# Kernel optimization log

Measured on AMD Instinct MI355X. Metric: run time of the kernel, lower is better.

The kernel has to match this reference:

```python
import jax, jax.numpy as jnp
import numpy as np

B, C, H, W = 8, 256, 64, 64
CR = C // 4  # reduced channels for Q/K


def setup_inputs() -> dict:
    key = jax.random.key(0)
    ks = jax.random.split(key, 6)
    return {
        "source": jax.random.normal(ks[0], (B, C, H, W), dtype=jnp.float32),
        "guidance": jax.random.normal(ks[1], (B, C, H, W), dtype=jnp.float32),
        "Wq": jax.random.normal(ks[2], (CR, C), dtype=jnp.float32) * 0.02,
        "Wk": jax.random.normal(ks[3], (CR, C), dtype=jnp.float32) * 0.02,
        "Wv": jax.random.normal(ks[4], (C, C), dtype=jnp.float32) * 0.02,
        "bv": jax.random.normal(ks[5], (C,), dtype=jnp.float32) * 0.02,
        "gamma": jnp.zeros((1,), dtype=jnp.float32),
    }


def reference(source, guidance, Wq, Wk, Wv, bv, gamma):
    b, c, h, w = source.shape
    n = h * w
    src = source.reshape(b, c, n)       # [B,C,N]
    gui = guidance.reshape(b, c, n)     # [B,C,N]
    # 1x1 convs == per-pixel linear projections over channels
    Q = jnp.einsum('qc,bcn->bqn', Wq, src)                 # [B,CR,N]
    K = jnp.einsum('qc,bcn->bqn', Wk, gui)                 # [B,CR,N]
    V = jnp.einsum('vc,bcn->bvn', Wv, gui) + bv[None, :, None]  # [B,C,N]
    # energy[b,n,m] = sum_q Q[b,q,n] K[b,q,m]  (unscaled)
    energy = jnp.einsum('bqn,bqm->bnm', Q, K)              # [B,N,N]
    attn = jax.nn.softmax(energy, axis=-1)                 # softmax over keys m
    # out[b,c,n] = sum_m V[b,c,m] attn[b,n,m]
    out = jnp.einsum('bcm,bnm->bcn', V, attn)              # [B,C,N]
    return gamma[0] * out.reshape(b, c, h, w) + source
```

## Files before the change

kernel.cpp:

```cpp
#include <hip/hip_runtime.h>
#include <hip/hip_bf16.h>
#include <stdint.h>


#define B_ 8
#define C_ 256
#define N_ 4096
#define CR_ 64

typedef unsigned short u16;
typedef __attribute__((ext_vector_type(8))) __bf16 bf16x8;
typedef __attribute__((ext_vector_type(4))) float f32x4;
typedef __attribute__((ext_vector_type(16))) float f32x16;

__device__ __forceinline__ u16 f2bf(float f) {
  union { float f; unsigned int u; } v; v.f = f;
  unsigned int r = (v.u + 0x7fffu + ((v.u >> 16) & 1u)) >> 16;
  return (u16)r;
}
__device__ __forceinline__ unsigned int cvtpk(float a, float b) {
  unsigned int r;
  asm("v_cvt_pk_bf16_f32 %0, %1, %2" : "=v"(r) : "v"(a), "v"(b));
  return r;
}

typedef __attribute__((address_space(1))) const unsigned int gu32_t;
typedef __attribute__((address_space(3))) unsigned int lu32_t;
__device__ __forceinline__ void gll16(const void* g, void* l) {
  __builtin_amdgcn_global_load_lds((gu32_t*)g, (lu32_t*)l, 16, 0, 0);
}

__global__ __launch_bounds__(256) void wprep_kernel(
    const float* __restrict__ Wq, const float* __restrict__ Wk,
    const float* __restrict__ Wv, u16* __restrict__ Wb)
{
  const int i = (blockIdx.x * 256 + threadIdx.x) * 4;
  const int row = i >> 8;
  float4 v;
  float s = 1.0f;
  if (row < 64)       { v = *(const float4*)(Wq + i); s = 1.44269504f; }
  else if (row < 128) { v = *(const float4*)(Wk + i - 64 * 256); }
  else                { v = *(const float4*)(Wv + i - 128 * 256); }
  u16* o = Wb + i;
  o[0] = f2bf(v.x * s); o[1] = f2bf(v.y * s);
  o[2] = f2bf(v.z * s); o[3] = f2bf(v.w * s);
}

#define TSTR 266
#define LOAD_TILE(INP, BB, PX0) do {                                         \
    const int p4_ = (t & 15) * 4, r_ = t >> 4;                               \
    const float* ip_ = (INP) + (size_t)(BB) * C_ * N_ + (PX0) + p4_;         \
    for (int k = 0; k < 16; ++k) {                                           \
      const int c_ = r_ + k * 16;                                            \
      float4 v_ = *(const float4*)(ip_ + (size_t)c_ * N_);                   \
      Tl[(p4_ + 0) * TSTR + c_] = f2bf(v_.x);                                \
      Tl[(p4_ + 1) * TSTR + c_] = f2bf(v_.y);                                \
      Tl[(p4_ + 2) * TSTR + c_] = f2bf(v_.z);                                \
      Tl[(p4_ + 3) * TSTR + c_] = f2bf(v_.w);                                \
    }                                                                        \
  } while (0)

__global__ __launch_bounds__(256) void projqk_kernel(
    const float* __restrict__ src, const float* __restrict__ gui,
    const u16* __restrict__ Wb, u16* __restrict__ Qb, u16* __restrict__ Kb)
{
  __shared__ u16 Tl[64 * TSTR];
  const int t = threadIdx.x, lane = t & 63, wave = t >> 6;
  const int lg = lane >> 4, lm = lane & 15;
  const int b = blockIdx.y;
  const int role = blockIdx.z;
  const float* in = role ? gui : src;
  const u16* W64 = Wb + role * 64 * 256;
  u16* dst = role ? Kb : Qb;

  LOAD_TILE(in, b, blockIdx.x * 64);
  __syncthreads();

  f32x4 acc[4];
  const f32x4 z4 = {0.f, 0.f, 0.f, 0.f};
#pragma unroll
  for (int i = 0; i < 4; ++i) acc[i] = z4;

  for (int ks = 0; ks < 8; ++ks) {
    bf16x8 wf = *(const bf16x8*)(W64 + (wave * 16 + lm) * C_ + ks * 32 + lg * 8);
#pragma unroll
    for (int ni = 0; ni < 4; ++ni) {
      bf16x8 pf = *(const bf16x8*)(&Tl[(ni * 16 + lm) * TSTR + ks * 32 + lg * 8]);
      acc[ni] = __builtin_amdgcn_mfma_f32_16x16x32_bf16(wf, pf, acc[ni], 0, 0, 0);
    }
  }
  __syncthreads();

#pragma unroll
  for (int ni = 0; ni < 4; ++ni)
#pragma unroll
    for (int rp = 0; rp < 2; ++rp)
      *(unsigned int*)&Tl[(ni * 16 + lm) * 72 + wave * 16 + lg * 4 + rp * 2] =
          cvtpk(acc[ni][rp * 2], acc[ni][rp * 2 + 1]);
  __syncthreads();

  const int l31 = lane & 31, hi2 = lane >> 5;
  const int tt = b * 64 + blockIdx.x;
  u16* op = dst + (size_t)tt * 4096 + lane * 8;
#pragma unroll
  for (int fi = 0; fi < 2; ++fi) {
    const int f = wave * 2 + fi, sub = f >> 2, db = f & 3;
    *(uint4*)(op + f * 512) =
        *(const uint4*)(&Tl[(sub * 32 + l31) * 72 + db * 16 + hi2 * 8]);
  }
}

__global__ __launch_bounds__(256) void projv_kernel(
    const float* __restrict__ gui, const u16* __restrict__ Wv256,
    const float* __restrict__ bv, u16* __restrict__ VF)
{
  __shared__ u16 Tl[64 * TSTR];
  const int t = threadIdx.x, lane = t & 63, wave = t >> 6;
  const int lg = lane >> 4, lm = lane & 15;
  const int b = blockIdx.y, half = blockIdx.z;

  LOAD_TILE(gui, b, blockIdx.x * 64);
  __syncthreads();

  const int chb = half * 128 + wave * 32;
  const u16* wb = Wv256 + (size_t)chb * C_;
  f32x4 acc[2][4];
  const f32x4 z4 = {0.f, 0.f, 0.f, 0.f};
#pragma unroll
  for (int i = 0; i < 2; ++i)
#pragma unroll
    for (int j = 0; j < 4; ++j) acc[i][j] = z4;

  for (int ks = 0; ks < 8; ++ks) {
    bf16x8 wf[2], pf[4];
#pragma unroll
    for (int mi = 0; mi < 2; ++mi)
      wf[mi] = *(const bf16x8*)(wb + (mi * 16 + lm) * C_ + ks * 32 + lg * 8);
#pragma unroll
    for (int ni = 0; ni < 4; ++ni)
      pf[ni] = *(const bf16x8*)(&Tl[(ni * 16 + lm) * TSTR + ks * 32 + lg * 8]);
#pragma unroll
    for (int mi = 0; mi < 2; ++mi)
#pragma unroll
      for (int ni = 0; ni < 4; ++ni)
        acc[mi][ni] = __builtin_amdgcn_mfma_f32_16x16x32_bf16(wf[mi], pf[ni], acc[mi][ni], 0, 0, 0);
  }

  f32x4 bq[2];
#pragma unroll
  for (int mi = 0; mi < 2; ++mi)
    bq[mi] = *(const f32x4*)(bv + chb + mi * 16 + lg * 4);

  __syncthreads();
  u16* tw = Tl + wave * 32 * 72;
#pragma unroll
  for (int mi = 0; mi < 2; ++mi)
#pragma unroll
    for (int ni = 0; ni < 4; ++ni)
#pragma unroll
      for (int r = 0; r < 4; ++r)
        tw[(mi * 16 + lg * 4 + r) * 72 + ni * 16 + lm] = f2bf(acc[mi][ni][r] + bq[mi][r]);

  const int l31 = lane & 31, hi2 = lane >> 5;
  u16* vo = VF + (((size_t)(b * 64 + blockIdx.x)) * 2 + half) * 8192;
#pragma unroll
  for (int kblk = 0; kblk < 4; ++kblk)
    *(uint4*)(vo + (wave * 4 + kblk) * 512 + lane * 8) =
        *(const uint4*)(&tw[l31 * 72 + kblk * 16 + hi2 * 8]);
}

#define VB1 16384
#define PB  32768

__global__ __launch_bounds__(256, 4) void attn_kernel(
    const u16* __restrict__ Qb, const u16* __restrict__ Kb, const u16* __restrict__ VF,
    const float* __restrict__ source, const float* __restrict__ gamma,
    float* __restrict__ out)
{
  __shared__ uint4 smem4[2560];
  char* smem = (char*)smem4;

  const int bid = blockIdx.x;
  const int b = bid & 7;
  const int idx = bid >> 3;
  const int qt = idx & 63;
  const int half = idx >> 6;

  const int t = threadIdx.x;
  const int lane = t & 63;
  const int wave = t >> 6;
  const int qw = wave & 1;
  const int wc = wave >> 1;
  const int l31 = lane & 31;
  const int hi = lane >> 5;
  const int q0 = qt * 64;

  bf16x8 aq[4];
  {
    const u16* qp = Qb + ((size_t)(b * 64 + qt)) * 4096 + (qw * 4) * 512 + lane * 8;
#pragma unroll
    for (int db = 0; db < 4; ++db) aq[db] = *(const bf16x8*)(qp + db * 512);
  }

  const u16* KbT = Kb + (size_t)b * (64 * 4096);
  const char* VFb = (const char*)VF + ((size_t)(b * 128 + half)) * 16384;

  f32x16 acc[2];
#pragma unroll
  for (int c2 = 0; c2 < 2; ++c2)
#pragma unroll
    for (int r = 0; r < 16; ++r) acc[c2][r] = 0.f;
  float lpart = 0.f;

  bf16x8 kC[4];
  char* pmy0 = smem + PB + (size_t)((qw * 4 + wc * 2 + 0) << 10) + lane * 16;
  char* pmy1 = smem + PB + (size_t)((qw * 4 + wc * 2 + 1) << 10) + lane * 16;
  const char* pfr0 = smem + PB + (size_t)((qw * 4 + (1 - wc) * 2 + 0) << 10) + lane * 16;
  const char* pfr1 = smem + PB + (size_t)((qw * 4 + (1 - wc) * 2 + 1) << 10) + lane * 16;

#define STAGEV(KTILE, VOFF) do {                                             \
    const char* vs_ = VFb + (size_t)(KTILE) * 32768 + t * 16;                \
    _Pragma("unroll")                                                        \
    for (int i = 0; i < 4; ++i)                                              \
      gll16(vs_ + i * 4096, smem + (VOFF) + wave * 1024 + i * 4096);         \
  } while (0)

#define LOADK(KT) do {                                                       \
    const u16* kp_ = KbT + (size_t)(KT) * 4096 + wc * 2048 + lane * 8;       \
    _Pragma("unroll")                                                        \
    for (int f = 0; f < 4; ++f)                                              \
      kC[f] = *(const bf16x8*)(kp_ + f * 512);                               \
  } while (0)

#define PACK(SF, O8, DST) do {                                               \
    unsigned uA_ = cvtpk(SF[(O8) + 0], SF[(O8) + 1]);                        \
    unsigned vA_ = cvtpk(SF[(O8) + 2], SF[(O8) + 3]);                        \
    unsigned uB_ = cvtpk(SF[(O8) + 4], SF[(O8) + 5]);                        \
    unsigned vB_ = cvtpk(SF[(O8) + 6], SF[(O8) + 7]);                        \
    asm("v_permlane32_swap_b32 %0, %1" : "+v"(uA_), "+v"(uB_));              \
    asm("v_permlane32_swap_b32 %0, %1" : "+v"(vA_), "+v"(vB_));              \
    uint4 pw_; pw_.x = uA_; pw_.y = vA_; pw_.z = uB_; pw_.w = vB_;           \
    __builtin_memcpy(&(DST), &pw_, 16);                                      \
  } while (0)

#define PVK(KBLK, PB8, VCUR) do {                                            \
    __builtin_amdgcn_s_setprio(1);                                           \
    _Pragma("unroll")                                                        \
    for (int c2 = 0; c2 < 2; ++c2) {                                         \
      bf16x8 vf_ = *(const bf16x8*)(smem + (VCUR) +                          \
          (((wc * 2 + c2) * 4 + (KBLK)) << 10) + lane * 16);                 \
      acc[c2] = __builtin_amdgcn_mfma_f32_32x32x16_bf16(vf_, PB8, acc[c2], 0, 0, 0); \
    }                                                                        \
    __builtin_amdgcn_s_setprio(0);                                           \
  } while (0)

#define ITER(KT, VCUR, VNXT) do {                                            \
    __syncthreads();                                                         \
    const int ktn_ = (KT) + 1;                                               \
    const bool ok_ = ktn_ < 64;                                              \
    if (ok_) STAGEV(ktn_, VNXT);                                             \
    f32x16 sf;                                                               \
    _Pragma("unroll")                                                        \
    for (int r = 0; r < 16; ++r) sf[r] = 0.f;                                \
    __builtin_amdgcn_s_setprio(1);                                           \
    _Pragma("unroll")                                                        \
    for (int db = 0; db < 4; ++db)                                           \
      sf = __builtin_amdgcn_mfma_f32_32x32x16_bf16(kC[db], aq[db], sf, 0, 0, 0); \
    __builtin_amdgcn_s_setprio(0);                                           \
    if (ok_) LOADK(ktn_);                                                    \
    float s_ = 0.f;                                                          \
    _Pragma("unroll")                                                        \
    for (int r = 0; r < 16; ++r) {                                           \
      float e_ = __builtin_amdgcn_exp2f(sf[r]);                              \
      sf[r] = e_;                                                            \
      s_ += e_;                                                              \
    }                                                                        \
    lpart += s_;                                                             \
    bf16x8 pf0_, pf1_;                                                       \
    PACK(sf, 0, pf0_);                                                       \
    PACK(sf, 8, pf1_);                                                       \
    *(uint4*)pmy0 = *(const uint4*)&pf0_;                                    \
    *(uint4*)pmy1 = *(const uint4*)&pf1_;                                    \
    asm volatile("s_waitcnt lgkmcnt(0)" ::: "memory");                       \
    __builtin_amdgcn_s_barrier();                                            \
    __builtin_amdgcn_sched_barrier(0);                                       \
    bf16x8 pfa_ = *(const bf16x8*)pfr0;                                      \
    bf16x8 pfb_ = *(const bf16x8*)pfr1;                                      \
    PVK(wc * 2 + 0, pf0_, VCUR);                                             \
    PVK(wc * 2 + 1, pf1_, VCUR);                                             \
    PVK((1 - wc) * 2 + 0, pfa_, VCUR);                                       \
    PVK((1 - wc) * 2 + 1, pfb_, VCUR);                                       \
  } while (0)

  STAGEV(0, 0);
  LOADK(0);
  for (int kt2 = 0; kt2 < 64; kt2 += 2) {
    ITER(kt2,     0,   VB1);
    ITER(kt2 + 1, VB1, 0);
  }
  asm volatile("s_waitcnt vmcnt(0)" ::: "memory");

  float xs = lpart, ys = lpart;
  asm("v_permlane32_swap_b32 %0, %1" : "+v"(xs), "+v"(ys));
  float lhalf = xs + ys;
  __syncthreads();
  *(float*)(smem + PB + (size_t)(((qw * 2 + wc) * 64 + lane) << 2)) = lhalf;
  __syncthreads();
  float lrow = lhalf +
      *(const float*)(smem + PB + (size_t)(((qw * 2 + (1 - wc)) * 64 + lane) << 2));

  const float inv = gamma[0] / fmaxf(lrow, 1e-37f);
#pragma unroll
  for (int c2 = 0; c2 < 2; ++c2)
#pragma unroll
    for (int r = 0; r < 16; ++r) {
      const int ch = half * 128 + wc * 64 + c2 * 32 + (r & 3) + 8 * (r >> 2) + 4 * hi;
      size_t gi = ((size_t)(b * C_ + ch)) * N_ + q0 + qw * 32 + l31;
      out[gi] = acc[c2][r] * inv + source[gi];
    }
}

extern "C" void kernel_launch(void* const* d_in, const int* in_sizes, int n_in,
                              void* d_out, int out_size, void* d_ws, size_t ws_size,
                              hipStream_t stream) {
  const float* src = (const float*)d_in[0];
  const float* gui = (const float*)d_in[1];
  const float* Wq  = (const float*)d_in[2];
  const float* Wk  = (const float*)d_in[3];
  const float* Wv  = (const float*)d_in[4];
  const float* bv  = (const float*)d_in[5];
  const float* gm  = (const float*)d_in[6];
  float* out = (float*)d_out;

  u16* Qb = (u16*)d_ws;
  u16* Kb = Qb + (size_t)B_ * N_ * CR_;
  u16* VF = Kb + (size_t)B_ * N_ * CR_;

  u16* Wb = (u16*)d_out;

  wprep_kernel<<<dim3(96), dim3(256), 0, stream>>>(Wq, Wk, Wv, Wb);
  projqk_kernel<<<dim3(64, B_, 2), dim3(256), 0, stream>>>(src, gui, Wb, Qb, Kb);
  projv_kernel<<<dim3(64, B_, 2), dim3(256), 0, stream>>>(gui, Wb + 128 * 256, bv, VF);
  attn_kernel<<<dim3(1024), dim3(256), 0, stream>>>(Qb, Kb, VF, src, gm, out);
}
```

Baseline: 155.4 us.

## Fuse K and V projections into one kernel sharing the guidance tile

Merges the Q/K projection kernel and the V projection kernel into one launch. Blocks with z=0 compute Q from source. Blocks with z=1 load the guidance tile once and compute both K and all 256 V channels from it. This removes the repeated fp32 reads and bf16 conversion of guidance across three block groups and drops one kernel launch. The cost is an imbalanced grid: the guidance blocks do roughly five times the MFMA work of the Q blocks and hold many more accumulator registers, which may lower occupancy.

Measured after the change: 155.0 us (median of 2 runs). No clear change (-0.2%).

```diff
diff --git a/kernel.cpp b/kernel.cpp
--- a/kernel.cpp
+++ b/kernel.cpp
@@ -60,113 +60,124 @@
     }                                                                        \
   } while (0)
 
-__global__ __launch_bounds__(256) void projqk_kernel(
+__global__ __launch_bounds__(256) void projqkv_kernel(
     const float* __restrict__ src, const float* __restrict__ gui,
-    const u16* __restrict__ Wb, u16* __restrict__ Qb, u16* __restrict__ Kb)
+    const u16* __restrict__ Wb, const float* __restrict__ bv,
+    u16* __restrict__ Qb, u16* __restrict__ Kb, u16* __restrict__ VF)
 {
   __shared__ u16 Tl[64 * TSTR];
   const int t = threadIdx.x, lane = t & 63, wave = t >> 6;
   const int lg = lane >> 4, lm = lane & 15;
   const int b = blockIdx.y;
-  const int role = blockIdx.z;
-  const float* in = role ? gui : src;
-  const u16* W64 = Wb + role * 64 * 256;
-  u16* dst = role ? Kb : Qb;
-
-  LOAD_TILE(in, b, blockIdx.x * 64);
-  __syncthreads();
-
-  f32x4 acc[4];
+  const int l31 = lane & 31, hi2 = lane >> 5;
   const f32x4 z4 = {0.f, 0.f, 0.f, 0.f};
-#pragma unroll
-  for (int i = 0; i < 4; ++i) acc[i] = z4;
-
-  for (int ks = 0; ks < 8; ++ks) {
-    bf16x8 wf = *(const bf16x8*)(W64 + (wave * 16 + lm) * C_ + ks * 32 + lg * 8);
-#pragma unroll
-    for (int ni = 0; ni < 4; ++ni) {
-      bf16x8 pf = *(const bf16x8*)(&Tl[(ni * 16 + lm) * TSTR + ks * 32 + lg * 8]);
-      acc[ni] = __builtin_amdgcn_mfma_f32_16x16x32_bf16(wf, pf, acc[ni], 0, 0, 0);
+
+  if (blockIdx.z == 0) {
+    LOAD_TILE(src, b, blockIdx.x * 64);
+    __syncthreads();
+
+    f32x4 acc[4];
+#pragma unroll
+    for (int i = 0; i < 4; ++i) acc[i] = z4;
+    for (int ks = 0; ks < 8; ++ks) {
+      bf16x8 wf = *(const bf16x8*)(Wb + (wave * 16 + lm) * C_ + ks * 32 + lg * 8);
+#pragma unroll
+      for (int ni = 0; ni < 4; ++ni) {
+        bf16x8 pf = *(const bf16x8*)(&Tl[(ni * 16 + lm) * TSTR + ks * 32 + lg * 8]);
+        acc[ni] = __builtin_amdgcn_mfma_f32_16x16x32_bf16(wf, pf, acc[ni], 0, 0, 0);
+      }
+    }
+    __syncthreads();
+#pragma unroll
+    for (int ni = 0; ni < 4; ++ni)
+#pragma unroll
+      for (int rp = 0; rp < 2; ++rp)
+        *(unsigned int*)&Tl[(ni * 16 + lm) * 72 + wave * 16 + lg * 4 + rp * 2] =
+            cvtpk(acc[ni][rp * 2], acc[ni][rp * 2 + 1]);
+    __syncthreads();
+    u16* op = Qb + (size_t)(b * 64 + blockIdx.x) * 4096 + lane * 8;
+#pragma unroll
+    for (int fi = 0; fi < 2; ++fi) {
+      const int f = wave * 2 + fi, sub = f >> 2, db = f & 3;
+      *(uint4*)(op + f * 512) =
+          *(const uint4*)(&Tl[(sub * 32 + l31) * 72 + db * 16 + hi2 * 8]);
+    }
+  } else {
+    LOAD_TILE(gui, b, blockIdx.x * 64);
+    __syncthreads();
+
+    const u16* Wk64 = Wb + 64 * 256;
+    const u16* Wv0  = Wb + 128 * 256 + (size_t)(wave * 64) * 256;
+    f32x4 acck[4];
+    f32x4 accv[4][4];
+#pragma unroll
+    for (int i = 0; i < 4; ++i) {
+      acck[i] = z4;
+#pragma unroll
+      for (int j = 0; j < 4; ++j) accv[i][j] = z4;
+    }
+
+    for (int ks = 0; ks < 8; ++ks) {
+      bf16x8 pf[4];
+#pragma unroll
+      for (int ni = 0; ni < 4; ++ni)
+        pf[ni] = *(const bf16x8*)(&Tl[(ni * 16 + lm) * TSTR + ks * 32 + lg * 8]);
+      bf16x8 kwf = *(const bf16x8*)(Wk64 + (wave * 16 + lm) * C_ + ks * 32 + lg * 8);
+#pragma unroll
+      for (int ni = 0; ni < 4; ++ni)
+        acck[ni] = __builtin_amdgcn_mfma_f32_16x16x32_bf16(kwf, pf[ni], acck[ni], 0, 0, 0);
+#pragma unroll
+      for (int mi = 0; mi < 4; ++mi) {
+        bf16x8 vwf = *(const bf16x8*)(Wv0 + (mi * 16 + lm) * C_ + ks * 32 + lg * 8);
+#pragma unroll
+        for (int ni = 0; ni < 4; ++ni)
+          accv[mi][ni] = __builtin_amdgcn_mfma_f32_16x16x32_bf16(vwf, pf[ni], accv[mi][ni], 0, 0, 0);
+      }
+    }
+
+    f32x4 bq[4];
+#pragma unroll
+    for (int mi = 0; mi < 4; ++mi)
+      bq[mi] = *(const f32x4*)(bv + wave * 64 + mi * 16 + lg * 4);
+
+    __syncthreads();
+
+    u16* tw = Tl + wave * 32 * 72;
+    const int half = wave >> 1;
+    u16* vo = VF + (((size_t)(b * 64 + blockIdx.x)) * 2 + half) * 8192;
+#pragma unroll
+    for (int vh = 0; vh < 2; ++vh) {
+#pragma unroll
+      for (int mi = 0; mi < 2; ++mi)
+#pragma unroll
+        for (int ni = 0; ni < 4; ++ni)
+#pragma unroll
+          for (int r = 0; r < 4; ++r)
+            tw[(mi * 16 + lg * 4 + r) * 72 + ni * 16 + lm] =
+                f2bf(accv[vh * 2 + mi][ni][r] + bq[vh * 2 + mi][r]);
+      const int cf = (wave & 1) * 2 + vh;
+#pragma unroll
+      for (int kblk = 0; kblk < 4; ++kblk)
+        *(uint4*)(vo + (cf * 4 + kblk) * 512 + lane * 8) =
+            *(const uint4*)(&tw[l31 * 72 + kblk * 16 + hi2 * 8]);
+    }
+
+    __syncthreads();
+#pragma unroll
+    for (int ni = 0; ni < 4; ++ni)
+#pragma unroll
+      for (int rp = 0; rp < 2; ++rp)
+        *(unsigned int*)&Tl[(ni * 16 + lm) * 72 + wave * 16 + lg * 4 + rp * 2] =
+            cvtpk(acck[ni][rp * 2], acck[ni][rp * 2 + 1]);
+    __syncthreads();
+    u16* op = Kb + (size_t)(b * 64 + blockIdx.x) * 4096 + lane * 8;
+#pragma unroll
+    for (int fi = 0; fi < 2; ++fi) {
+      const int f = wave * 2 + fi, sub = f >> 2, db = f & 3;
+      *(uint4*)(op + f * 512) =
+          *(const uint4*)(&Tl[(sub * 32 + l31) * 72 + db * 16 + hi2 * 8]);
     }
   }
-  __syncthreads();
-
-#pragma unroll
-  for (int ni = 0; ni < 4; ++ni)
-#pragma unroll
-    for (int rp = 0; rp < 2; ++rp)
-      *(unsigned int*)&Tl[(ni * 16 + lm) * 72 + wave * 16 + lg * 4 + rp * 2] =
-          cvtpk(acc[ni][rp * 2], acc[ni][rp * 2 + 1]);
-  __syncthreads();
-
-  const int l31 = lane & 31, hi2 = lane >> 5;
-  const int tt = b * 64 + blockIdx.x;
-  u16* op = dst + (size_t)tt * 4096 + lane * 8;
-#pragma unroll
-  for (int fi = 0; fi < 2; ++fi) {
-    const int f = wave * 2 + fi, sub = f >> 2, db = f & 3;
-    *(uint4*)(op + f * 512) =
-        *(const uint4*)(&Tl[(sub * 32 + l31) * 72 + db * 16 + hi2 * 8]);
-  }
-}
-
-__global__ __launch_bounds__(256) void projv_kernel(
-    const float* __restrict__ gui, const u16* __restrict__ Wv256,
-    const float* __restrict__ bv, u16* __restrict__ VF)
-{
-  __shared__ u16 Tl[64 * TSTR];
-  const int t = threadIdx.x, lane = t & 63, wave = t >> 6;
-  const int lg = lane >> 4, lm = lane & 15;
-  const int b = blockIdx.y, half = blockIdx.z;
-
-  LOAD_TILE(gui, b, blockIdx.x * 64);
-  __syncthreads();
-
-  const int chb = half * 128 + wave * 32;
-  const u16* wb = Wv256 + (size_t)chb * C_;
-  f32x4 acc[2][4];
-  const f32x4 z4 = {0.f, 0.f, 0.f, 0.f};
-#pragma unroll
-  for (int i = 0; i < 2; ++i)
-#pragma unroll
-    for (int j = 0; j < 4; ++j) acc[i][j] = z4;
-
-  for (int ks = 0; ks < 8; ++ks) {
-    bf16x8 wf[2], pf[4];
-#pragma unroll
-    for (int mi = 0; mi < 2; ++mi)
-      wf[mi] = *(const bf16x8*)(wb + (mi * 16 + lm) * C_ + ks * 32 + lg * 8);
-#pragma unroll
-    for (int ni = 0; ni < 4; ++ni)
-      pf[ni] = *(const bf16x8*)(&Tl[(ni * 16 + lm) * TSTR + ks * 32 + lg * 8]);
-#pragma unroll
-    for (int mi = 0; mi < 2; ++mi)
-#pragma unroll
-      for (int ni = 0; ni < 4; ++ni)
-        acc[mi][ni] = __builtin_amdgcn_mfma_f32_16x16x32_bf16(wf[mi], pf[ni], acc[mi][ni], 0, 0, 0);
-  }
-
-  f32x4 bq[2];
-#pragma unroll
-  for (int mi = 0; mi < 2; ++mi)
-    bq[mi] = *(const f32x4*)(bv + chb + mi * 16 + lg * 4);
-
-  __syncthreads();
-  u16* tw = Tl + wave * 32 * 72;
-#pragma unroll
-  for (int mi = 0; mi < 2; ++mi)
-#pragma unroll
-    for (int ni = 0; ni < 4; ++ni)
-#pragma unroll
-      for (int r = 0; r < 4; ++r)
-        tw[(mi * 16 + lg * 4 + r) * 72 + ni * 16 + lm] = f2bf(acc[mi][ni][r] + bq[mi][r]);
-
-  const int l31 = lane & 31, hi2 = lane >> 5;
-  u16* vo = VF + (((size_t)(b * 64 + blockIdx.x)) * 2 + half) * 8192;
-#pragma unroll
-  for (int kblk = 0; kblk < 4; ++kblk)
-    *(uint4*)(vo + (wave * 4 + kblk) * 512 + lane * 8) =
-        *(const uint4*)(&tw[l31 * 72 + kblk * 16 + hi2 * 8]);
 }
 
 #define VB1 16384
@@ -339,7 +350,6 @@
   u16* Wb = (u16*)d_out;
 
   wprep_kernel<<<dim3(96), dim3(256), 0, stream>>>(Wq, Wk, Wv, Wb);
-  projqk_kernel<<<dim3(64, B_, 2), dim3(256), 0, stream>>>(src, gui, Wb, Qb, Kb);
-  projv_kernel<<<dim3(64, B_, 2), dim3(256), 0, stream>>>(gui, Wb + 128 * 256, bv, VF);
+  projqkv_kernel<<<dim3(64, B_, 2), dim3(256), 0, stream>>>(src, gui, Wb, bv, Qb, Kb, VF);
   attn_kernel<<<dim3(1024), dim3(256), 0, stream>>>(Qb, Kb, VF, src, gm, out);
 }
```
